# Kernel optimization log

Measured on AMD Instinct MI355X. Metric: run time of the kernel, lower is better.

Reference implementation:

```python
import jax, jax.numpy as jnp
import numpy as np

THETA = 0.5
STRIDE = 2
HEADS = 4
D_K = 32
D_V = 32
EPS = 1e-5


def pdc_conv(x, w, stride, theta=THETA):
    """Conv_PDC: (Co,Ci,1,8) weight -> 3x3 kernel with zero center, minus theta * 1x1 sum conv."""
    Co, Ci = w.shape[0], w.shape[1]
    w8 = w[:, :, 0, :]  # (Co, Ci, 8)
    w9 = jnp.concatenate(
        [w8[:, :, :4], jnp.zeros((Co, Ci, 1), w.dtype), w8[:, :, 4:]], axis=2
    ).reshape(Co, Ci, 3, 3)
    dn = jax.lax.conv_dimension_numbers(x.shape, w9.shape, ('NCHW', 'OIHW', 'NCHW'))
    out_n = jax.lax.conv_general_dilated(x, w9, (stride, stride), [(1, 1), (1, 1)], dimension_numbers=dn)
    kd = jnp.sum(w8, axis=2)[:, :, None, None]  # (Co, Ci, 1, 1)
    out_d = jax.lax.conv_general_dilated(x, kd, (stride, stride), [(0, 0), (0, 0)], dimension_numbers=dn)
    return out_n - theta * out_d


def full_layer_norm(x):
    # F.layer_norm(x, x.shape): normalize over ALL dims (incl. batch), no affine
    m = jnp.mean(x)
    v = jnp.mean(jnp.square(x - m))
    return (x - m) * jax.lax.rsqrt(v + EPS)


def setup_inputs() -> dict:
    key = jax.random.key(0)
    ks = jax.random.split(key, 12)
    b, c, h, w = 8, 64, 64, 64
    hd = HEADS * D_K  # 128
    s = 0.05
    return {
        'x': jax.random.normal(ks[0], (b, c, h, w), jnp.float32),
        'wk': jax.random.normal(ks[1], (c, c, 1, 8), jnp.float32) * s,
        'wv': jax.random.normal(ks[2], (c, c, 1, 8), jnp.float32) * s,
        'fcq_w': jax.random.normal(ks[3], (hd, c), jnp.float32) * s,
        'fcq_b': jax.random.normal(ks[4], (hd,), jnp.float32) * s,
        'fck_w': jax.random.normal(ks[5], (hd, c), jnp.float32) * s,
        'fck_b': jax.random.normal(ks[6], (hd,), jnp.float32) * s,
        'fcv_w': jax.random.normal(ks[7], (hd, c), jnp.float32) * s,
        'fcv_b': jax.random.normal(ks[8], (hd,), jnp.float32) * s,
        'fco_w': jax.random.normal(ks[9], (c, hd), jnp.float32) * s,
        'fco_b': jax.random.normal(ks[10], (c,), jnp.float32) * s,
        'B': jax.random.normal(ks[11], (1, HEADS, h * w, (h // STRIDE) * (w // STRIDE)), jnp.float32) * s,
    }


def reference(x, wk, wv, fcq_w, fcq_b, fck_w, fck_b, fcv_w, fcv_b, fco_w, fco_b, B):
    b, c, h, w = x.shape
    hw = h * w
    xr = jnp.transpose(x.reshape(b, c, hw), (0, 2, 1))  # (b, hw, c)
    xr = full_layer_norm(xr)

    q = xr @ fcq_w.T + fcq_b                    # (b, hw, H*dk)
    q = jnp.transpose(q.reshape(b, hw, HEADS, D_K), (0, 2, 1, 3))  # (b,H,hw,dk)

    k = pdc_conv(x, wk, STRIDE)                 # (b, c, h2, w2)
    kb, kc, kh, kw = k.shape
    k = jnp.transpose(k.reshape(kb, kc, kh * kw), (0, 2, 1)) @ fck_w.T + fck_b
    k = jnp.transpose(k.reshape(kb, kh * kw, HEADS, D_K), (0, 2, 1, 3))  # (b,H,n2,dk)

    v = pdc_conv(x, wv, STRIDE)
    vb, vc, vh, vw = v.shape
    v = jnp.transpose(v.reshape(vb, vc, vh * vw), (0, 2, 1)) @ fcv_w.T + fcv_b
    v = jnp.transpose(v.reshape(vb, vh * vw, HEADS, D_V), (0, 2, 1, 3))  # (b,H,n2,dv)

    attn = jnp.einsum('bhid,bhjd->bhij', q, k) * (D_K ** -0.5) + B
    attn = jax.nn.softmax(attn, axis=-1)
    out = jnp.einsum('bhij,bhjd->bhid', attn, v)            # (b,H,hw,dv)
    out = jnp.transpose(out, (0, 2, 1, 3)).reshape(b, hw, HEADS * D_V)
    out = out @ fco_w.T + fco_b                              # (b, hw, c)
    # Faithful to source: .view(b, channels, h, w) without permute
    out = out.reshape(b, c, h, w)
    return out + x
```

## Files before the change

kernel.cpp:

```cpp
#include <hip/hip_runtime.h>
#include <cmath>

#define THETA 0.5f
#define EPS 1e-5f

typedef __attribute__((ext_vector_type(8))) short bf16x8;
typedef __attribute__((ext_vector_type(4))) float f32x4;
typedef __attribute__((ext_vector_type(4))) unsigned u32x4;

__device__ inline unsigned short f2b(float f) {
  unsigned u = __builtin_bit_cast(unsigned, f);
  return (unsigned short)((u + 0x7fffu + ((u >> 16) & 1u)) >> 16);
}
__device__ inline float b2f(unsigned short u) {
  unsigned v = (unsigned)u << 16;
  return __builtin_bit_cast(float, v);
}
__device__ inline float blo(unsigned u) { return __builtin_bit_cast(float, u << 16); }
__device__ inline float bhi(unsigned u) { return __builtin_bit_cast(float, u & 0xffff0000u); }
__device__ inline float exp2fast(float x) {
  float r;
  asm("v_exp_f32 %0, %1" : "=v"(r) : "v"(x));
  return r;
}

__global__ __launch_bounds__(256) void pre_kernel(
    const float* __restrict__ B, unsigned short* __restrict__ B2, int nB4,
    const float* __restrict__ x, float* __restrict__ stats, int nx4) {
  int bx = blockIdx.x;
  if (bx < 2048) {
    int tid = bx * 256 + threadIdx.x;
    int stride = 2048 * 256;
    const float4* b4 = (const float4*)B;
    const float L = 1.4426950408889634f;
    for (int i = tid; i < nB4; i += stride) {
      float4 v = b4[i];
      unsigned lo = f2b(v.x * L) | ((unsigned)f2b(v.y * L) << 16);
      unsigned hi = f2b(v.z * L) | ((unsigned)f2b(v.w * L) << 16);
      *(uint2*)(B2 + (size_t)i * 4) = make_uint2(lo, hi);
    }
  } else {
    int sb = bx - 2048;
    int tid = sb * 256 + threadIdx.x;
    int stride = 512 * 256;
    float s = 0.f, ss = 0.f;
    const float4* x4 = (const float4*)x;
    for (int i = tid; i < nx4; i += stride) {
      float4 v = x4[i];
      s  += v.x + v.y + v.z + v.w;
      ss += v.x * v.x + v.y * v.y + v.z * v.z + v.w * v.w;
    }
    for (int off = 32; off; off >>= 1) {
      s  += __shfl_down(s, off);
      ss += __shfl_down(ss, off);
    }
    __shared__ float ls[4], lss[4];
    int lane = threadIdx.x & 63, wid = threadIdx.x >> 6;
    if (lane == 0) { ls[wid] = s; lss[wid] = ss; }
    __syncthreads();
    if (threadIdx.x == 0) {
      float a = 0.f, b = 0.f;
      for (int w = 0; w < 4; ++w) { a += ls[w]; b += lss[w]; }
      stats[2 * sb]     = a;
      stats[2 * sb + 1] = b;
    }
  }
}

__global__ __launch_bounds__(256) void pdc_conv_kernel(
    const float* __restrict__ x,
    const float* __restrict__ wk,
    const float* __restrict__ wv,
    float* __restrict__ Kc,
    float* __restrict__ Vc) {
  int oh  = blockIdx.x;
  int coh = blockIdx.y;
  int bb  = blockIdx.z;
  __shared__ float xs[64][3][64];
  const float* xb = x + (size_t)bb * 262144;
  int r1 = 2 * oh;
  for (int i = 0; i < 48; ++i) {
    int idx = threadIdx.x + i * 256;
    int ci = idx / 192;
    int rem = idx - ci * 192;
    int r = rem >> 6, col = rem & 63;
    int row = r1 - 1 + r;
    xs[ci][r][col] = (row >= 0) ? xb[((size_t)ci * 64 + row) * 64 + col] : 0.f;
  }
  __syncthreads();
  int owl = threadIdx.x & 7;
  int co  = coh * 32 + (threadIdx.x >> 3);
  int c0 = owl * 8;
  int ecol = c0 ? c0 - 1 : 0;
  float accK[4] = {0.f, 0.f, 0.f, 0.f}, accV[4] = {0.f, 0.f, 0.f, 0.f};
  const float* wkc = wk + (size_t)co * 512;
  const float* wvc = wv + (size_t)co * 512;
  for (int ci = 0; ci < 64; ++ci) {
    float4 k0 = *(const float4*)(wkc + ci * 8);
    float4 k1 = *(const float4*)(wkc + ci * 8 + 4);
    float4 v0 = *(const float4*)(wvc + ci * 8);
    float4 v1 = *(const float4*)(wvc + ci * 8 + 4);
    float kdk = k0.x + k0.y + k0.z + k0.w + k1.x + k1.y + k1.z + k1.w;
    float kdv = v0.x + v0.y + v0.z + v0.w + v1.x + v1.y + v1.z + v1.w;
    float wK[9] = {k0.x, k0.y, k0.z, k0.w, -THETA * kdk, k1.x, k1.y, k1.z, k1.w};
    float wV[9] = {v0.x, v0.y, v0.z, v0.w, -THETA * kdv, v1.x, v1.y, v1.z, v1.w};
    float xr[3][9];
#pragma unroll
    for (int r = 0; r < 3; ++r) {
      float ev = owl ? xs[ci][r][ecol] : 0.f;
      float4 a = *(const float4*)&xs[ci][r][c0];
      float4 b = *(const float4*)&xs[ci][r][c0 + 4];
      xr[r][0] = ev;
      xr[r][1] = a.x; xr[r][2] = a.y; xr[r][3] = a.z; xr[r][4] = a.w;
      xr[r][5] = b.x; xr[r][6] = b.y; xr[r][7] = b.z; xr[r][8] = b.w;
    }
#pragma unroll
    for (int ky = 0; ky < 3; ++ky)
#pragma unroll
      for (int kx = 0; kx < 3; ++kx) {
        float wkk = wK[ky * 3 + kx], wvv = wV[ky * 3 + kx];
#pragma unroll
        for (int i = 0; i < 4; ++i) {
          float xv = xr[ky][2 * i + kx];
          accK[i] = fmaf(wkk, xv, accK[i]);
          accV[i] = fmaf(wvv, xv, accV[i]);
        }
      }
  }
  size_t o = ((size_t)bb * 64 + co) * 1024 + oh * 32 + owl * 4;
  *(float4*)&Kc[o] = make_float4(accK[0], accK[1], accK[2], accK[3]);
  *(float4*)&Vc[o] = make_float4(accV[0], accV[1], accV[2], accV[3]);
}

__device__ inline void proj_body(
    const float* __restrict__ A, const float* __restrict__ W,
    const float* __restrict__ bias, unsigned short* __restrict__ out,
    const float* __restrict__ stats, int R, int doLN, int transp,
    int r0, int h, int bb) {
  float m = 0.f, rs = 1.f;
  if (doLN) {
    const float2* sp = (const float2*)stats;
    float2 a = sp[threadIdx.x];
    float2 b2 = sp[threadIdx.x + 256];
    float s = a.x + b2.x, ss = a.y + b2.y;
    for (int off = 32; off; off >>= 1) {
      s  += __shfl_down(s, off);
      ss += __shfl_down(ss, off);
    }
    __shared__ float red[8];
    int lane0 = threadIdx.x & 63, wid0 = threadIdx.x >> 6;
    if (lane0 == 0) { red[wid0] = s; red[4 + wid0] = ss; }
    __syncthreads();
    float ts  = red[0] + red[1] + red[2] + red[3];
    float tss = red[4] + red[5] + red[6] + red[7];
    const float inv = 1.0f / 2097152.0f;
    m = ts * inv;
    float v = tss * inv - m * m;
    rs = rsqrtf(v + EPS);
    __syncthreads();
  }
  __shared__ float As[64][64];
  const float* Ab = A + (size_t)bb * 64 * R;
  for (int i = 0; i < 16; ++i) {
    int idx = threadIdx.x + i * 256;
    int c = idx >> 6, rr = idx & 63;
    float v = Ab[(size_t)c * R + r0 + rr];
    if (doLN) v = (v - m) * rs;
    As[c][rr] = v;
  }
  __syncthreads();
  int lane = threadIdx.x & 63;
  int w = __builtin_amdgcn_readfirstlane(threadIdx.x >> 6);
  int dbase = h * 32 + w * 8;
  float acc[8];
#pragma unroll
  for (int i = 0; i < 8; ++i) acc[i] = bias[dbase + i];
  for (int c = 0; c < 64; ++c) {
    float a = As[c][lane];
#pragma unroll
    for (int i = 0; i < 8; ++i)
      acc[i] = fmaf(a, W[(size_t)(dbase + i) * 64 + c], acc[i]);
  }
  size_t bh = (size_t)bb * 4 + h;
  if (!transp) {
    unsigned p0 = f2b(acc[0]) | ((unsigned)f2b(acc[1]) << 16);
    unsigned p1 = f2b(acc[2]) | ((unsigned)f2b(acc[3]) << 16);
    unsigned p2 = f2b(acc[4]) | ((unsigned)f2b(acc[5]) << 16);
    unsigned p3 = f2b(acc[6]) | ((unsigned)f2b(acc[7]) << 16);
    *(uint4*)(out + (bh * R + r0 + lane) * 32 + w * 8) = make_uint4(p0, p1, p2, p3);
  } else {
#pragma unroll
    for (int i = 0; i < 8; ++i)
      out[(bh * 32 + w * 8 + i) * (size_t)R + r0 + lane] = f2b(acc[i]);
  }
}

__global__ __launch_bounds__(256) void proj_all_kernel(
    const float* __restrict__ x, const float* __restrict__ Kc, const float* __restrict__ Vc,
    const float* __restrict__ Wq, const float* __restrict__ bq,
    const float* __restrict__ Wk, const float* __restrict__ bk,
    const float* __restrict__ Wv, const float* __restrict__ bv,
    unsigned short* __restrict__ Qb, unsigned short* __restrict__ Kb,
    unsigned short* __restrict__ Vtb, const float* __restrict__ stats) {
  int bx = blockIdx.x;
  if (bx < 2048) {
    int r0 = (bx & 63) * 64, h = (bx >> 6) & 3, bb = bx >> 8;
    proj_body(x, Wq, bq, Qb, stats, 4096, 1, 0, r0, h, bb);
  } else {
    int i = bx - 2048;
    int r0 = (i & 15) * 64, h = (i >> 4) & 3, bb = (i >> 6) & 7, kv = i >> 9;
    proj_body(kv ? Vc : Kc, kv ? Wv : Wk, kv ? bv : bk, kv ? Vtb : Kb,
              (const float*)nullptr, 1024, 0, kv, r0, h, bb);
  }
}

__global__ __launch_bounds__(256, 4) void attn_mfma_kernel(
    const unsigned short* __restrict__ Qb,
    const unsigned short* __restrict__ Kb,
    const unsigned short* __restrict__ Vtb,
    const unsigned short* __restrict__ B2,
    unsigned short* __restrict__ Ob) {
  int qt = blockIdx.x;
  int b  = blockIdx.y & 7;
  int h  = blockIdx.y >> 3;
  int tid = threadIdx.x;
  int w = tid >> 6, lane = tid & 63, g = lane >> 4, li = lane & 15;

  __shared__ __align__(16) unsigned short Ks[4096];
  __shared__ __align__(16) unsigned short Vs[4096];

  size_t bh = (size_t)b * 4 + h;
  int q0 = qt * 128 + w * 32;
  bf16x8 qfA = *(const bf16x8*)(Qb + (bh * 4096 + q0 + li) * 32 + g * 8);
  bf16x8 qfB = *(const bf16x8*)(Qb + (bh * 4096 + q0 + 16 + li) * 32 + g * 8);
  const unsigned short* BpA = B2 + ((size_t)h * 4096 + q0 + li) * 1024;
  const unsigned short* BpB = BpA + 16 * 1024;
  const unsigned short* Kg = Kb + bh * 32768;
  const unsigned short* Vg = Vtb + bh * 32768;

  float rsumA = 0.f, rsumB = 0.f;
  f32x4 accA0 = {0.f, 0.f, 0.f, 0.f}, accA1 = {0.f, 0.f, 0.f, 0.f};
  f32x4 accB0 = {0.f, 0.f, 0.f, 0.f}, accB1 = {0.f, 0.f, 0.f, 0.f};
  const float scale2 = 0.17677669529663687f * 1.4426950408889634f;

  int krow = tid >> 1, khalf = tid & 1;
  int j5 = krow & 31;
  int jp = (krow & ~31) | (((j5 >> 2) & 1) << 4) | (((j5 >> 3) & 3) << 2) | (j5 & 3);
  const int kc0 = ((jp >> 4) * 64 + khalf * 32 + (jp & 15)) * 8;
  int vr = tid >> 3, sg = tid & 7;
  const int vc0 = (((sg >> 1) * 2 + (vr >> 4)) * 64 + (sg & 1) * 32 + (vr & 15)) * 8;

  for (int jc = 0; jc < 1024; jc += 128) {
    __syncthreads();
    {
      const uint4* ks = (const uint4*)(Kg + (size_t)(jc + krow) * 32 + khalf * 16);
      *(uint4*)&Ks[kc0]       = ks[0];
      *(uint4*)&Ks[kc0 + 128] = ks[1];
      const uint4* vs = (const uint4*)(Vg + (size_t)vr * 1024 + jc + sg * 16);
      *(uint4*)&Vs[vc0]       = vs[0];
      *(uint4*)&Vs[vc0 + 128] = vs[1];
    }
    __syncthreads();

#pragma unroll
    for (int js = 0; js < 4; ++js) {
      bf16x8 kf0 = *(const bf16x8*)&Ks[((js * 2) * 64 + lane) * 8];
      bf16x8 kf1 = *(const bf16x8*)&Ks[((js * 2 + 1) * 64 + lane) * 8];
      const f32x4 z = {0.f, 0.f, 0.f, 0.f};
      f32x4 sA0 = __builtin_amdgcn_mfma_f32_16x16x32_bf16(kf0, qfA, z, 0, 0, 0);
      f32x4 sB0 = __builtin_amdgcn_mfma_f32_16x16x32_bf16(kf0, qfB, z, 0, 0, 0);
      f32x4 sA1 = __builtin_amdgcn_mfma_f32_16x16x32_bf16(kf1, qfA, z, 0, 0, 0);
      f32x4 sB1 = __builtin_amdgcn_mfma_f32_16x16x32_bf16(kf1, qfB, z, 0, 0, 0);

      u32x4 bA = *(const u32x4*)(BpA + jc + js * 32 + g * 8);
      u32x4 bB = *(const u32x4*)(BpB + jc + js * 32 + g * 8);

      float pA[8], pB[8];
      pA[0] = exp2fast(fmaf(sA0[0], scale2, blo(bA[0])));
      pA[1] = exp2fast(fmaf(sA0[1], scale2, bhi(bA[0])));
      pA[2] = exp2fast(fmaf(sA0[2], scale2, blo(bA[1])));
      pA[3] = exp2fast(fmaf(sA0[3], scale2, bhi(bA[1])));
      pA[4] = exp2fast(fmaf(sA1[0], scale2, blo(bA[2])));
      pA[5] = exp2fast(fmaf(sA1[1], scale2, bhi(bA[2])));
      pA[6] = exp2fast(fmaf(sA1[2], scale2, blo(bA[3])));
      pA[7] = exp2fast(fmaf(sA1[3], scale2, bhi(bA[3])));
      pB[0] = exp2fast(fmaf(sB0[0], scale2, blo(bB[0])));
      pB[1] = exp2fast(fmaf(sB0[1], scale2, bhi(bB[0])));
      pB[2] = exp2fast(fmaf(sB0[2], scale2, blo(bB[1])));
      pB[3] = exp2fast(fmaf(sB0[3], scale2, bhi(bB[1])));
      pB[4] = exp2fast(fmaf(sB1[0], scale2, blo(bB[2])));
      pB[5] = exp2fast(fmaf(sB1[1], scale2, bhi(bB[2])));
      pB[6] = exp2fast(fmaf(sB1[2], scale2, blo(bB[3])));
      pB[7] = exp2fast(fmaf(sB1[3], scale2, bhi(bB[3])));

      rsumA += ((pA[0] + pA[1]) + (pA[2] + pA[3])) + ((pA[4] + pA[5]) + (pA[6] + pA[7]));
      rsumB += ((pB[0] + pB[1]) + (pB[2] + pB[3])) + ((pB[4] + pB[5]) + (pB[6] + pB[7]));

      u32x4 wA, wB;
      asm("v_cvt_pk_bf16_f32 %0, %1, %2" : "=v"(wA[0]) : "v"(pA[0]), "v"(pA[1]));
      asm("v_cvt_pk_bf16_f32 %0, %1, %2" : "=v"(wA[1]) : "v"(pA[2]), "v"(pA[3]));
      asm("v_cvt_pk_bf16_f32 %0, %1, %2" : "=v"(wA[2]) : "v"(pA[4]), "v"(pA[5]));
      asm("v_cvt_pk_bf16_f32 %0, %1, %2" : "=v"(wA[3]) : "v"(pA[6]), "v"(pA[7]));
      asm("v_cvt_pk_bf16_f32 %0, %1, %2" : "=v"(wB[0]) : "v"(pB[0]), "v"(pB[1]));
      asm("v_cvt_pk_bf16_f32 %0, %1, %2" : "=v"(wB[1]) : "v"(pB[2]), "v"(pB[3]));
      asm("v_cvt_pk_bf16_f32 %0, %1, %2" : "=v"(wB[2]) : "v"(pB[4]), "v"(pB[5]));
      asm("v_cvt_pk_bf16_f32 %0, %1, %2" : "=v"(wB[3]) : "v"(pB[6]), "v"(pB[7]));
      bf16x8 paA = __builtin_bit_cast(bf16x8, wA);
      bf16x8 paB = __builtin_bit_cast(bf16x8, wB);

      bf16x8 vf0 = *(const bf16x8*)&Vs[(js * 128 + lane) * 8];
      bf16x8 vf1 = *(const bf16x8*)&Vs[((js * 2 + 1) * 64 + lane) * 8];
      accA0 = __builtin_amdgcn_mfma_f32_16x16x32_bf16(paA, vf0, accA0, 0, 0, 0);
      accA1 = __builtin_amdgcn_mfma_f32_16x16x32_bf16(paA, vf1, accA1, 0, 0, 0);
      accB0 = __builtin_amdgcn_mfma_f32_16x16x32_bf16(paB, vf0, accB0, 0, 0, 0);
      accB1 = __builtin_amdgcn_mfma_f32_16x16x32_bf16(paB, vf1, accB1, 0, 0, 0);
    }
  }

  rsumA += __shfl_xor(rsumA, 16);
  rsumA += __shfl_xor(rsumA, 32);
  rsumB += __shfl_xor(rsumB, 16);
  rsumB += __shfl_xor(rsumB, 32);
  float invA = 1.0f / rsumA;
  float invB = 1.0f / rsumB;
  float invqA[4], invqB[4];
#pragma unroll
  for (int r = 0; r < 4; ++r) {
    invqA[r] = __shfl(invA, g * 4 + r);
    invqB[r] = __shfl(invB, g * 4 + r);
  }

#pragma unroll
  for (int r = 0; r < 4; ++r) {
    size_t rowA = (size_t)b * 4096 + q0 + g * 4 + r;
    Ob[rowA * 128 + h * 32 + li]      = f2b(accA0[r] * invqA[r]);
    Ob[rowA * 128 + h * 32 + 16 + li] = f2b(accA1[r] * invqA[r]);
    size_t rowB = rowA + 16;
    Ob[rowB * 128 + h * 32 + li]      = f2b(accB0[r] * invqB[r]);
    Ob[rowB * 128 + h * 32 + 16 + li] = f2b(accB1[r] * invqB[r]);
  }
}

__global__ __launch_bounds__(256) void outproj_kernel(
    const unsigned short* __restrict__ O,
    const float* __restrict__ Wo,
    const float* __restrict__ bo,
    const float* __restrict__ x,
    float* __restrict__ out) {
  int r0 = blockIdx.x * 64;
  int bb = blockIdx.y;
  __shared__ float Os[128][65];
  const unsigned short* Obp = O + ((size_t)bb * 4096 + r0) * 128;
  for (int i = 0; i < 32; ++i) {
    int idx = threadIdx.x + i * 256;
    int e = idx & 127, rr = idx >> 7;
    Os[e][rr] = b2f(Obp[(size_t)rr * 128 + e]);
  }
  __syncthreads();
  int lane = threadIdx.x & 63;
  int w = __builtin_amdgcn_readfirstlane(threadIdx.x >> 6);
  float acc[16];
#pragma unroll
  for (int i = 0; i < 16; ++i) acc[i] = bo[w * 16 + i];
  for (int e = 0; e < 128; ++e) {
    float a = Os[e][lane];
#pragma unroll
    for (int i = 0; i < 16; ++i)
      acc[i] = fmaf(a, Wo[(size_t)(w * 16 + i) * 128 + e], acc[i]);
  }
  size_t base = (size_t)bb * 262144 + (size_t)(r0 + lane) * 64 + w * 16;
  const float* xp = x + base;
  float* op = out + base;
#pragma unroll
  for (int i = 0; i < 16; ++i) op[i] = acc[i] + xp[i];
}

extern "C" void kernel_launch(void* const* d_in, const int* in_sizes, int n_in,
                              void* d_out, int out_size, void* d_ws, size_t ws_size,
                              hipStream_t stream) {
  const float* x    = (const float*)d_in[0];
  const float* wk   = (const float*)d_in[1];
  const float* wv   = (const float*)d_in[2];
  const float* fcqw = (const float*)d_in[3];
  const float* fcqb = (const float*)d_in[4];
  const float* fckw = (const float*)d_in[5];
  const float* fckb = (const float*)d_in[6];
  const float* fcvw = (const float*)d_in[7];
  const float* fcvb = (const float*)d_in[8];
  const float* fcow = (const float*)d_in[9];
  const float* fcob = (const float*)d_in[10];
  const float* Bb   = (const float*)d_in[11];
  float* out = (float*)d_out;
  float* ws  = (float*)d_ws;

  float* stats = ws;
  float* Kc = ws + 1024;
  float* Vc = Kc + 524288;
  unsigned short* B2  = (unsigned short*)(Vc + 524288);
  unsigned short* Qb  = B2 + 16777216;
  unsigned short* Kb  = Qb + 4194304;
  unsigned short* Vtb = Kb + 1048576;
  unsigned short* Ob  = Vtb + 1048576;

  pre_kernel<<<dim3(2560), dim3(256), 0, stream>>>(Bb, B2, 4194304, x, stats, 524288);
  pdc_conv_kernel<<<dim3(32, 2, 8), dim3(256), 0, stream>>>(x, wk, wv, Kc, Vc);
  proj_all_kernel<<<dim3(3072), dim3(256), 0, stream>>>(
      x, Kc, Vc, fcqw, fcqb, fckw, fckb, fcvw, fcvb, Qb, Kb, Vtb, stats);
  attn_mfma_kernel<<<dim3(32, 32), dim3(256), 0, stream>>>(Qb, Kb, Vtb, B2, Ob);
  outproj_kernel<<<dim3(64, 8), dim3(256), 0, stream>>>(Ob, fcow, fcob, x, out);
}
```

Baseline: 256.8 us.

## Use MFMA for projections and read fp32 bias directly in attention

The Q/K/V projection and output projection kernels are rewritten to use bf16 MFMA instructions instead of scalar FMA loops, with weights converted to bf16 fragments in registers. The separate pre-pass that converted the large B bias to bf16 is removed, and attention now reads the fp32 bias directly and scales it inline. This avoids one full read and write of the bias, but doubles the bias bytes the attention kernel reads each pass and lowers projection precision to bf16 inputs.

```diff
diff --git a/kernel.cpp b/kernel.cpp
--- a/kernel.cpp
+++ b/kernel.cpp
@@ -16,54 +16,42 @@
   unsigned v = (unsigned)u << 16;
   return __builtin_bit_cast(float, v);
 }
-__device__ inline float blo(unsigned u) { return __builtin_bit_cast(float, u << 16); }
-__device__ inline float bhi(unsigned u) { return __builtin_bit_cast(float, u & 0xffff0000u); }
 __device__ inline float exp2fast(float x) {
   float r;
   asm("v_exp_f32 %0, %1" : "=v"(r) : "v"(x));
   return r;
 }
-
-__global__ __launch_bounds__(256) void pre_kernel(
-    const float* __restrict__ B, unsigned short* __restrict__ B2, int nB4,
-    const float* __restrict__ x, float* __restrict__ stats, int nx4) {
-  int bx = blockIdx.x;
-  if (bx < 2048) {
-    int tid = bx * 256 + threadIdx.x;
-    int stride = 2048 * 256;
-    const float4* b4 = (const float4*)B;
-    const float L = 1.4426950408889634f;
-    for (int i = tid; i < nB4; i += stride) {
-      float4 v = b4[i];
-      unsigned lo = f2b(v.x * L) | ((unsigned)f2b(v.y * L) << 16);
-      unsigned hi = f2b(v.z * L) | ((unsigned)f2b(v.w * L) << 16);
-      *(uint2*)(B2 + (size_t)i * 4) = make_uint2(lo, hi);
-    }
-  } else {
-    int sb = bx - 2048;
-    int tid = sb * 256 + threadIdx.x;
-    int stride = 512 * 256;
-    float s = 0.f, ss = 0.f;
-    const float4* x4 = (const float4*)x;
-    for (int i = tid; i < nx4; i += stride) {
-      float4 v = x4[i];
-      s  += v.x + v.y + v.z + v.w;
-      ss += v.x * v.x + v.y * v.y + v.z * v.z + v.w * v.w;
-    }
-    for (int off = 32; off; off >>= 1) {
-      s  += __shfl_down(s, off);
-      ss += __shfl_down(ss, off);
-    }
-    __shared__ float ls[4], lss[4];
-    int lane = threadIdx.x & 63, wid = threadIdx.x >> 6;
-    if (lane == 0) { ls[wid] = s; lss[wid] = ss; }
-    __syncthreads();
-    if (threadIdx.x == 0) {
-      float a = 0.f, b = 0.f;
-      for (int w = 0; w < 4; ++w) { a += ls[w]; b += lss[w]; }
-      stats[2 * sb]     = a;
-      stats[2 * sb + 1] = b;
-    }
+__device__ inline unsigned cvtpk(float lo, float hi) {
+  unsigned r;
+  asm("v_cvt_pk_bf16_f32 %0, %1, %2" : "=v"(r) : "v"(lo), "v"(hi));
+  return r;
+}
+
+__global__ __launch_bounds__(256) void stats_kernel(const float* __restrict__ x,
+                                                    float* __restrict__ stats, int nx4) {
+  int sb = blockIdx.x;
+  int tid = sb * 256 + threadIdx.x;
+  int stride = 512 * 256;
+  float s = 0.f, ss = 0.f;
+  const float4* x4 = (const float4*)x;
+  for (int i = tid; i < nx4; i += stride) {
+    float4 v = x4[i];
+    s  += v.x + v.y + v.z + v.w;
+    ss += v.x * v.x + v.y * v.y + v.z * v.z + v.w * v.w;
+  }
+  for (int off = 32; off; off >>= 1) {
+    s  += __shfl_down(s, off);
+    ss += __shfl_down(ss, off);
+  }
+  __shared__ float ls[4], lss[4];
+  int lane = threadIdx.x & 63, wid = threadIdx.x >> 6;
+  if (lane == 0) { ls[wid] = s; lss[wid] = ss; }
+  __syncthreads();
+  if (threadIdx.x == 0) {
+    float a = 0.f, b = 0.f;
+    for (int w = 0; w < 4; ++w) { a += ls[w]; b += lss[w]; }
+    stats[2 * sb]     = a;
+    stats[2 * sb + 1] = b;
   }
 }
 
@@ -132,23 +120,40 @@
   *(float4*)&Vc[o] = make_float4(accV[0], accV[1], accV[2], accV[3]);
 }
 
-__device__ inline void proj_body(
-    const float* __restrict__ A, const float* __restrict__ W,
-    const float* __restrict__ bias, unsigned short* __restrict__ out,
-    const float* __restrict__ stats, int R, int doLN, int transp,
-    int r0, int h, int bb) {
+__global__ __launch_bounds__(256) void proj_mfma_kernel(
+    const float* __restrict__ x, const float* __restrict__ Kc, const float* __restrict__ Vc,
+    const float* __restrict__ Wq, const float* __restrict__ bq,
+    const float* __restrict__ Wk, const float* __restrict__ bk,
+    const float* __restrict__ Wv, const float* __restrict__ bv,
+    unsigned short* __restrict__ Qb, unsigned short* __restrict__ Kb,
+    unsigned short* __restrict__ Vtb, const float* __restrict__ stats) {
+  int bx = blockIdx.x;
+  const float* A; const float* W; const float* bias; unsigned short* outp;
+  int R, doLN, transp, r0, bb;
+  if (bx < 256) {
+    A = x; W = Wq; bias = bq; outp = Qb; R = 4096; doLN = 1; transp = 0;
+    bb = bx >> 5; r0 = (bx & 31) * 128;
+  } else {
+    int i = bx - 256; int kv = i >> 6; int j = i & 63;
+    bb = j >> 3; r0 = (j & 7) * 128; R = 1024; doLN = 0;
+    if (!kv) { A = Kc; W = Wk; bias = bk; outp = Kb;  transp = 0; }
+    else     { A = Vc; W = Wv; bias = bv; outp = Vtb; transp = 1; }
+  }
+  int tid = threadIdx.x;
+  int w = tid >> 6, lane = tid & 63, g = lane >> 4, li = lane & 15;
+
   float m = 0.f, rs = 1.f;
   if (doLN) {
     const float2* sp = (const float2*)stats;
-    float2 a = sp[threadIdx.x];
-    float2 b2 = sp[threadIdx.x + 256];
+    float2 a = sp[tid];
+    float2 b2 = sp[tid + 256];
     float s = a.x + b2.x, ss = a.y + b2.y;
     for (int off = 32; off; off >>= 1) {
       s  += __shfl_down(s, off);
       ss += __shfl_down(ss, off);
     }
     __shared__ float red[8];
-    int lane0 = threadIdx.x & 63, wid0 = threadIdx.x >> 6;
+    int lane0 = tid & 63, wid0 = tid >> 6;
     if (lane0 == 0) { red[wid0] = s; red[4 + wid0] = ss; }
     __syncthreads();
     float ts  = red[0] + red[1] + red[2] + red[3];
@@ -159,58 +164,84 @@
     rs = rsqrtf(v + EPS);
     __syncthreads();
   }
-  __shared__ float As[64][64];
+
+  bf16x8 wf[2][2];
+#pragma unroll
+  for (int dd = 0; dd < 2; ++dd)
+#pragma unroll
+    for (int kh = 0; kh < 2; ++kh) {
+      const float* wp = W + (size_t)(w * 32 + dd * 16 + li) * 64 + kh * 32 + g * 8;
+      float4 w0 = *(const float4*)wp;
+      float4 w1 = *(const float4*)(wp + 4);
+      u32x4 u;
+      u[0] = cvtpk(w0.x, w0.y); u[1] = cvtpk(w0.z, w0.w);
+      u[2] = cvtpk(w1.x, w1.y); u[3] = cvtpk(w1.z, w1.w);
+      wf[dd][kh] = __builtin_bit_cast(bf16x8, u);
+    }
+
+  __shared__ __align__(16) unsigned short As2[128][72];
   const float* Ab = A + (size_t)bb * 64 * R;
-  for (int i = 0; i < 16; ++i) {
-    int idx = threadIdx.x + i * 256;
-    int c = idx >> 6, rr = idx & 63;
-    float v = Ab[(size_t)c * R + r0 + rr];
+  for (int i = 0; i < 32; ++i) {
+    int idx = tid + i * 256;
+    int c = idx >> 7, r = idx & 127;
+    float v = Ab[(size_t)c * R + r0 + r];
     if (doLN) v = (v - m) * rs;
-    As[c][rr] = v;
+    As2[r][c] = f2b(v);
   }
   __syncthreads();
-  int lane = threadIdx.x & 63;
-  int w = __builtin_amdgcn_readfirstlane(threadIdx.x >> 6);
-  int dbase = h * 32 + w * 8;
-  float acc[8];
-#pragma unroll
-  for (int i = 0; i < 8; ++i) acc[i] = bias[dbase + i];
-  for (int c = 0; c < 64; ++c) {
-    float a = As[c][lane];
-#pragma unroll
-    for (int i = 0; i < 8; ++i)
-      acc[i] = fmaf(a, W[(size_t)(dbase + i) * 64 + c], acc[i]);
-  }
-  size_t bh = (size_t)bb * 4 + h;
+
+  f32x4 acc[2][8];
+#pragma unroll
+  for (int dd = 0; dd < 2; ++dd)
+#pragma unroll
+    for (int rt = 0; rt < 8; ++rt) acc[dd][rt] = (f32x4){0.f, 0.f, 0.f, 0.f};
+
+#pragma unroll
+  for (int rt = 0; rt < 8; ++rt) {
+    bf16x8 xf0 = *(const bf16x8*)&As2[rt * 16 + li][g * 8];
+    bf16x8 xf1 = *(const bf16x8*)&As2[rt * 16 + li][32 + g * 8];
+    if (!transp) {
+#pragma unroll
+      for (int dd = 0; dd < 2; ++dd) {
+        acc[dd][rt] = __builtin_amdgcn_mfma_f32_16x16x32_bf16(wf[dd][0], xf0, acc[dd][rt], 0, 0, 0);
+        acc[dd][rt] = __builtin_amdgcn_mfma_f32_16x16x32_bf16(wf[dd][1], xf1, acc[dd][rt], 0, 0, 0);
+      }
+    } else {
+#pragma unroll
+      for (int dd = 0; dd < 2; ++dd) {
+        acc[dd][rt] = __builtin_amdgcn_mfma_f32_16x16x32_bf16(xf0, wf[dd][0], acc[dd][rt], 0, 0, 0);
+        acc[dd][rt] = __builtin_amdgcn_mfma_f32_16x16x32_bf16(xf1, wf[dd][1], acc[dd][rt], 0, 0, 0);
+      }
+    }
+  }
+
+  size_t bh = (size_t)bb * 4 + w;
   if (!transp) {
-    unsigned p0 = f2b(acc[0]) | ((unsigned)f2b(acc[1]) << 16);
-    unsigned p1 = f2b(acc[2]) | ((unsigned)f2b(acc[3]) << 16);
-    unsigned p2 = f2b(acc[4]) | ((unsigned)f2b(acc[5]) << 16);
-    unsigned p3 = f2b(acc[6]) | ((unsigned)f2b(acc[7]) << 16);
-    *(uint4*)(out + (bh * R + r0 + lane) * 32 + w * 8) = make_uint4(p0, p1, p2, p3);
+#pragma unroll
+    for (int dd = 0; dd < 2; ++dd) {
+      float4 b4 = *(const float4*)(bias + w * 32 + dd * 16 + g * 4);
+#pragma unroll
+      for (int rt = 0; rt < 8; ++rt) {
+        f32x4 a = acc[dd][rt];
+        unsigned lo = cvtpk(a[0] + b4.x, a[1] + b4.y);
+        unsigned hi = cvtpk(a[2] + b4.z, a[3] + b4.w);
+        int r = r0 + rt * 16 + li;
+        *(uint2*)(outp + (bh * R + r) * 32 + dd * 16 + g * 4) = make_uint2(lo, hi);
+      }
+    }
   } else {
 #pragma unroll
-    for (int i = 0; i < 8; ++i)
-      out[(bh * 32 + w * 8 + i) * (size_t)R + r0 + lane] = f2b(acc[i]);
-  }
-}
-
-__global__ __launch_bounds__(256) void proj_all_kernel(
-    const float* __restrict__ x, const float* __restrict__ Kc, const float* __restrict__ Vc,
-    const float* __restrict__ Wq, const float* __restrict__ bq,
-    const float* __restrict__ Wk, const float* __restrict__ bk,
-    const float* __restrict__ Wv, const float* __restrict__ bv,
-    unsigned short* __restrict__ Qb, unsigned short* __restrict__ Kb,
-    unsigned short* __restrict__ Vtb, const float* __restrict__ stats) {
-  int bx = blockIdx.x;
-  if (bx < 2048) {
-    int r0 = (bx & 63) * 64, h = (bx >> 6) & 3, bb = bx >> 8;
-    proj_body(x, Wq, bq, Qb, stats, 4096, 1, 0, r0, h, bb);
-  } else {
-    int i = bx - 2048;
-    int r0 = (i & 15) * 64, h = (i >> 4) & 3, bb = (i >> 6) & 7, kv = i >> 9;
-    proj_body(kv ? Vc : Kc, kv ? Wv : Wk, kv ? bv : bk, kv ? Vtb : Kb,
-              (const float*)nullptr, 1024, 0, kv, r0, h, bb);
+    for (int dd = 0; dd < 2; ++dd) {
+      float bsc = bias[w * 32 + dd * 16 + li];
+#pragma unroll
+      for (int rt = 0; rt < 8; ++rt) {
+        f32x4 a = acc[dd][rt];
+        unsigned lo = cvtpk(a[0] + bsc, a[1] + bsc);
+        unsigned hi = cvtpk(a[2] + bsc, a[3] + bsc);
+        *(uint2*)(outp + (bh * 32 + dd * 16 + li) * (size_t)R + r0 + rt * 16 + g * 4) =
+            make_uint2(lo, hi);
+      }
+    }
   }
 }
 
@@ -218,7 +249,7 @@
     const unsigned short* __restrict__ Qb,
     const unsigned short* __restrict__ Kb,
     const unsigned short* __restrict__ Vtb,
-    const unsigned short* __restrict__ B2,
+    const float* __restrict__ Bf,
     unsigned short* __restrict__ Ob) {
   int qt = blockIdx.x;
   int b  = blockIdx.y & 7;
@@ -233,14 +264,15 @@
   int q0 = qt * 128 + w * 32;
   bf16x8 qfA = *(const bf16x8*)(Qb + (bh * 4096 + q0 + li) * 32 + g * 8);
   bf16x8 qfB = *(const bf16x8*)(Qb + (bh * 4096 + q0 + 16 + li) * 32 + g * 8);
-  const unsigned short* BpA = B2 + ((size_t)h * 4096 + q0 + li) * 1024;
-  const unsigned short* BpB = BpA + 16 * 1024;
+  const float* BpA = Bf + ((size_t)h * 4096 + q0 + li) * 1024;
+  const float* BpB = BpA + 16 * 1024;
   const unsigned short* Kg = Kb + bh * 32768;
   const unsigned short* Vg = Vtb + bh * 32768;
 
   float rsumA = 0.f, rsumB = 0.f;
   f32x4 accA0 = {0.f, 0.f, 0.f, 0.f}, accA1 = {0.f, 0.f, 0.f, 0.f};
   f32x4 accB0 = {0.f, 0.f, 0.f, 0.f}, accB1 = {0.f, 0.f, 0.f, 0.f};
+  const float L = 1.4426950408889634f;
   const float scale2 = 0.17677669529663687f * 1.4426950408889634f;
 
   int krow = tid >> 1, khalf = tid & 1;
@@ -272,39 +304,37 @@
       f32x4 sA1 = __builtin_amdgcn_mfma_f32_16x16x32_bf16(kf1, qfA, z, 0, 0, 0);
       f32x4 sB1 = __builtin_amdgcn_mfma_f32_16x16x32_bf16(kf1, qfB, z, 0, 0, 0);
 
-      u32x4 bA = *(const u32x4*)(BpA + jc + js * 32 + g * 8);
-      u32x4 bB = *(const u32x4*)(BpB + jc + js * 32 + g * 8);
+      float4 a0 = *(const float4*)(BpA + jc + js * 32 + g * 8);
+      float4 a1 = *(const float4*)(BpA + jc + js * 32 + g * 8 + 4);
+      float4 c0 = *(const float4*)(BpB + jc + js * 32 + g * 8);
+      float4 c1 = *(const float4*)(BpB + jc + js * 32 + g * 8 + 4);
 
       float pA[8], pB[8];
-      pA[0] = exp2fast(fmaf(sA0[0], scale2, blo(bA[0])));
-      pA[1] = exp2fast(fmaf(sA0[1], scale2, bhi(bA[0])));
-      pA[2] = exp2fast(fmaf(sA0[2], scale2, blo(bA[1])));
-      pA[3] = exp2fast(fmaf(sA0[3], scale2, bhi(bA[1])));
-      pA[4] = exp2fast(fmaf(sA1[0], scale2, blo(bA[2])));
-      pA[5] = exp2fast(fmaf(sA1[1], scale2, bhi(bA[2])));
-      pA[6] = exp2fast(fmaf(sA1[2], scale2, blo(bA[3])));
-      pA[7] = exp2fast(fmaf(sA1[3], scale2, bhi(bA[3])));
-      pB[0] = exp2fast(fmaf(sB0[0], scale2, blo(bB[0])));
-      pB[1] = exp2fast(fmaf(sB0[1], scale2, bhi(bB[0])));
-      pB[2] = exp2fast(fmaf(sB0[2], scale2, blo(bB[1])));
-      pB[3] = exp2fast(fmaf(sB0[3], scale2, bhi(bB[1])));
-      pB[4] = exp2fast(fmaf(sB1[0], scale2, blo(bB[2])));
-      pB[5] = exp2fast(fmaf(sB1[1], scale2, bhi(bB[2])));
-      pB[6] = exp2fast(fmaf(sB1[2], scale2, blo(bB[3])));
-      pB[7] = exp2fast(fmaf(sB1[3], scale2, bhi(bB[3])));
+      pA[0] = exp2fast(fmaf(sA0[0], scale2, a0.x * L));
+      pA[1] = exp2fast(fmaf(sA0[1], scale2, a0.y * L));
+      pA[2] = exp2fast(fmaf(sA0[2], scale2, a0.z * L));
+      pA[3] = exp2fast(fmaf(sA0[3], scale2, a0.w * L));
+      pA[4] = exp2fast(fmaf(sA1[0], scale2, a1.x * L));
+      pA[5] = exp2fast(fmaf(sA1[1], scale2, a1.y * L));
+      pA[6] = exp2fast(fmaf(sA1[2], scale2, a1.z * L));
+      pA[7] = exp2fast(fmaf(sA1[3], scale2, a1.w * L));
+      pB[0] = exp2fast(fmaf(sB0[0], scale2, c0.x * L));
+      pB[1] = exp2fast(fmaf(sB0[1], scale2, c0.y * L));
+      pB[2] = exp2fast(fmaf(sB0[2], scale2, c0.z * L));
+      pB[3] = exp2fast(fmaf(sB0[3], scale2, c0.w * L));
+      pB[4] = exp2fast(fmaf(sB1[0], scale2, c1.x * L));
+      pB[5] = exp2fast(fmaf(sB1[1], scale2, c1.y * L));
+      pB[6] = exp2fast(fmaf(sB1[2], scale2, c1.z * L));
+      pB[7] = exp2fast(fmaf(sB1[3], scale2, c1.w * L));
 
       rsumA += ((pA[0] + pA[1]) + (pA[2] + pA[3])) + ((pA[4] + pA[5]) + (pA[6] + pA[7]));
       rsumB += ((pB[0] + pB[1]) + (pB[2] + pB[3])) + ((pB[4] + pB[5]) + (pB[6] + pB[7]));
 
       u32x4 wA, wB;
-      asm("v_cvt_pk_bf16_f32 %0, %1, %2" : "=v"(wA[0]) : "v"(pA[0]), "v"(pA[1]));
-      asm("v_cvt_pk_bf16_f32 %0, %1, %2" : "=v"(wA[1]) : "v"(pA[2]), "v"(pA[3]));
-      asm("v_cvt_pk_bf16_f32 %0, %1, %2" : "=v"(wA[2]) : "v"(pA[4]), "v"(pA[5]));
-      asm("v_cvt_pk_bf16_f32 %0, %1, %2" : "=v"(wA[3]) : "v"(pA[6]), "v"(pA[7]));
-      asm("v_cvt_pk_bf16_f32 %0, %1, %2" : "=v"(wB[0]) : "v"(pB[0]), "v"(pB[1]));
-      asm("v_cvt_pk_bf16_f32 %0, %1, %2" : "=v"(wB[1]) : "v"(pB[2]), "v"(pB[3]));
-      asm("v_cvt_pk_bf16_f32 %0, %1, %2" : "=v"(wB[2]) : "v"(pB[4]), "v"(pB[5]));
-      asm("v_cvt_pk_bf16_f32 %0, %1, %2" : "=v"(wB[3]) : "v"(pB[6]), "v"(pB[7]));
+      wA[0] = cvtpk(pA[0], pA[1]); wA[1] = cvtpk(pA[2], pA[3]);
+      wA[2] = cvtpk(pA[4], pA[5]); wA[3] = cvtpk(pA[6], pA[7]);
+      wB[0] = cvtpk(pB[0], pB[1]); wB[1] = cvtpk(pB[2], pB[3]);
+      wB[2] = cvtpk(pB[4], pB[5]); wB[3] = cvtpk(pB[6], pB[7]);
       bf16x8 paA = __builtin_bit_cast(bf16x8, wA);
       bf16x8 paB = __builtin_bit_cast(bf16x8, wB);
 
@@ -341,38 +371,60 @@
   }
 }
 
-__global__ __launch_bounds__(256) void outproj_kernel(
+__global__ __launch_bounds__(256) void outproj_mfma_kernel(
     const unsigned short* __restrict__ O,
     const float* __restrict__ Wo,
     const float* __restrict__ bo,
     const float* __restrict__ x,
     float* __restrict__ out) {
-  int r0 = blockIdx.x * 64;
-  int bb = blockIdx.y;
-  __shared__ float Os[128][65];
-  const unsigned short* Obp = O + ((size_t)bb * 4096 + r0) * 128;
-  for (int i = 0; i < 32; ++i) {
-    int idx = threadIdx.x + i * 256;
-    int e = idx & 127, rr = idx >> 7;
-    Os[e][rr] = b2f(Obp[(size_t)rr * 128 + e]);
-  }
-  __syncthreads();
-  int lane = threadIdx.x & 63;
-  int w = __builtin_amdgcn_readfirstlane(threadIdx.x >> 6);
-  float acc[16];
-#pragma unroll
-  for (int i = 0; i < 16; ++i) acc[i] = bo[w * 16 + i];
-  for (int e = 0; e < 128; ++e) {
-    float a = Os[e][lane];
-#pragma unroll
-    for (int i = 0; i < 16; ++i)
-      acc[i] = fmaf(a, Wo[(size_t)(w * 16 + i) * 128 + e], acc[i]);
-  }
-  size_t base = (size_t)bb * 262144 + (size_t)(r0 + lane) * 64 + w * 16;
-  const float* xp = x + base;
-  float* op = out + base;
-#pragma unroll
-  for (int i = 0; i < 16; ++i) op[i] = acc[i] + xp[i];
+  int pb = blockIdx.x & 31;
+  int bb = blockIdx.x >> 5;
+  int tid = threadIdx.x;
+  int w = tid >> 6, lane = tid & 63, g = lane >> 4, li = lane & 15;
+  int p0 = pb * 128;
+
+  bf16x8 wf[4];
+#pragma unroll
+  for (int kt = 0; kt < 4; ++kt) {
+    const float* wp = Wo + (size_t)(w * 16 + li) * 128 + kt * 32 + g * 8;
+    float4 w0 = *(const float4*)wp;
+    float4 w1 = *(const float4*)(wp + 4);
+    u32x4 u;
+    u[0] = cvtpk(w0.x, w0.y); u[1] = cvtpk(w0.z, w0.w);
+    u[2] = cvtpk(w1.x, w1.y); u[3] = cvtpk(w1.z, w1.w);
+    wf[kt] = __builtin_bit_cast(bf16x8, u);
+  }
+
+  f32x4 acc[8];
+#pragma unroll
+  for (int pt = 0; pt < 8; ++pt) acc[pt] = (f32x4){0.f, 0.f, 0.f, 0.f};
+
+#pragma unroll
+  for (int pt = 0; pt < 8; ++pt) {
+    const unsigned short* Op = O + ((size_t)bb * 4096 + p0 + pt * 16 + li) * 128;
+    bf16x8 of0 = *(const bf16x8*)(Op + g * 8);
+    bf16x8 of1 = *(const bf16x8*)(Op + 32 + g * 8);
+    bf16x8 of2 = *(const bf16x8*)(Op + 64 + g * 8);
+    bf16x8 of3 = *(const bf16x8*)(Op + 96 + g * 8);
+    acc[pt] = __builtin_amdgcn_mfma_f32_16x16x32_bf16(wf[0], of0, acc[pt], 0, 0, 0);
+    acc[pt] = __builtin_amdgcn_mfma_f32_16x16x32_bf16(wf[1], of1, acc[pt], 0, 0, 0);
+    acc[pt] = __builtin_amdgcn_mfma_f32_16x16x32_bf16(wf[2], of2, acc[pt], 0, 0, 0);
+    acc[pt] = __builtin_amdgcn_mfma_f32_16x16x32_bf16(wf[3], of3, acc[pt], 0, 0, 0);
+  }
+
+  float4 bo4 = *(const float4*)(bo + w * 16 + g * 4);
+#pragma unroll
+  for (int pt = 0; pt < 8; ++pt) {
+    int p = p0 + pt * 16 + li;
+    size_t base = (size_t)bb * 262144 + (size_t)p * 64 + w * 16 + g * 4;
+    float4 xr = *(const float4*)(x + base);
+    float4 o;
+    o.x = acc[pt][0] + bo4.x + xr.x;
+    o.y = acc[pt][1] + bo4.y + xr.y;
+    o.z = acc[pt][2] + bo4.z + xr.z;
+    o.w = acc[pt][3] + bo4.w + xr.w;
+    *(float4*)(out + base) = o;
+  }
 }
 
 extern "C" void kernel_launch(void* const* d_in, const int* in_sizes, int n_in,
@@ -396,16 +448,15 @@
   float* stats = ws;
   float* Kc = ws + 1024;
   float* Vc = Kc + 524288;
-  unsigned short* B2  = (unsigned short*)(Vc + 524288);
-  unsigned short* Qb  = B2 + 16777216;
+  unsigned short* Qb  = (unsigned short*)(Vc + 524288);
   unsigned short* Kb  = Qb + 4194304;
   unsigned short* Vtb = Kb + 1048576;
   unsigned short* Ob  = Vtb + 1048576;
 
-  pre_kernel<<<dim3(2560), dim3(256), 0, stream>>>(Bb, B2, 4194304, x, stats, 524288);
+  stats_kernel<<<dim3(512), dim3(256), 0, stream>>>(x, stats, 524288);
   pdc_conv_kernel<<<dim3(32, 2, 8), dim3(256), 0, stream>>>(x, wk, wv, Kc, Vc);
-  proj_all_kernel<<<dim3(3072), dim3(256), 0, stream>>>(
+  proj_mfma_kernel<<<dim3(384), dim3(256), 0, stream>>>(
       x, Kc, Vc, fcqw, fcqb, fckw, fckb, fcvw, fcvb, Qb, Kb, Vtb, stats);
-  attn_mfma_kernel<<<dim3(32, 32), dim3(256), 0, stream>>>(Qb, Kb, Vtb, B2, Ob);
-  outproj_kernel<<<dim3(64, 8), dim3(256), 0, stream>>>(Ob, fcow, fcob, x, out);
-}
+  attn_mfma_kernel<<<dim3(32, 32), dim3(256), 0, stream>>>(Qb, Kb, Vtb, Bb, Ob);
+  outproj_mfma_kernel<<<dim3(256), dim3(256), 0, stream>>>(Ob, fcow, fcob, x, out);
+}
```

Measured after the change: 243.7 us. 1.05x faster.
